# Kernel tuning notes

Hardware: AMD Instinct MI355X
Metric: run time of the kernel (lower is better)

## Reference

```python
import jax, jax.numpy as jnp
import numpy as np
from jax import lax

LENGTH, WIDTH = 64, 64
INPUT_DIM = 1


def _convlstm_layer(x_tbchw, W, b):
    """Run one ConvLSTM layer over time. x_tbchw: (L,B,Cin,H,W).
    W: (4*hid, Cin+hid, 3, 3), b: (4*hid,). Returns (outputs (L,B,hid,H,W), last_h)."""
    L, B, _, H, Wd = x_tbchw.shape
    hid = W.shape[0] // 4
    h0 = jnp.zeros((B, hid, H, Wd), dtype=x_tbchw.dtype)
    c0 = jnp.zeros((B, hid, H, Wd), dtype=x_tbchw.dtype)

    def step(carry, xt):
        h, c = carry
        z = lax.conv_general_dilated(
            jnp.concatenate([xt, h], axis=1), W,
            window_strides=(1, 1), padding='SAME',
            dimension_numbers=('NCHW', 'OIHW', 'NCHW'))
        z = z + b[None, :, None, None]
        cc_i, cc_f, cc_o, cc_g = jnp.split(z, 4, axis=1)
        c_next = jax.nn.sigmoid(cc_f) * c + jax.nn.sigmoid(cc_i) * jnp.tanh(cc_g)
        h_next = jax.nn.sigmoid(cc_o) * jnp.tanh(c_next)
        return (h_next, c_next), h_next

    (h_last, _), outs = lax.scan(step, (h0, c0), x_tbchw)
    return outs, h_last


def setup_inputs() -> dict:
    key = jax.random.key(0)
    k1, k2, k3 = jax.random.split(key, 3)
    B, L, N = 16, 12, LENGTH * WIDTH
    emd, out_len = 128, 12
    return {
        'history_data': jax.random.normal(k1, (B, L, N, 1), dtype=jnp.float32),
        'future_data': jnp.zeros((B, L, N, 1), dtype=jnp.float32),
        'W0': jax.random.normal(k2, (4 * emd, INPUT_DIM + emd, 3, 3), dtype=jnp.float32) * 0.05,
        'b0': jnp.zeros((4 * emd,), dtype=jnp.float32),
        'W1': jax.random.normal(k3, (4 * out_len, emd + out_len, 3, 3), dtype=jnp.float32) * 0.05,
        'b1': jnp.zeros((4 * out_len,), dtype=jnp.float32),
        'batch_seen': 0,
        'epoch': 0,
        'train': 1,
    }


def reference(history_data, future_data, W0, b0, W1, b1, batch_seen, epoch, train):
    B, L, N, C = history_data.shape
    # (B,L,1,H,W) -> (L,B,1,H,W) for time-major scan
    x = history_data[..., :INPUT_DIM].reshape(B, L, INPUT_DIM, LENGTH, WIDTH)
    x = jnp.transpose(x, (1, 0, 2, 3, 4))
    outs0, _ = _convlstm_layer(x, W0, b0)          # (L,B,emd,H,W)
    _, h_last = _convlstm_layer(outs0, W1, b1)     # (B,out_len,H,W)
    prediction = h_last.reshape(B, L, LENGTH * WIDTH)[..., None]  # (B,L,N,1)
    return prediction
```

## Files before the change

kernel.cpp:

```cpp
#include <hip/hip_runtime.h>
#include <hip/hip_bf16.h>


typedef __attribute__((ext_vector_type(8))) short short8;
typedef __attribute__((ext_vector_type(4))) float float4v;

#define CS 160
#define KTOT 1440
#define RSTR 2560
#define BSTR 10240

__device__ __forceinline__ float sigf(float x) { return 1.f / (1.f + __expf(-x)); }
__device__ __forceinline__ short f2hs(float v) {
  _Float16 h = (_Float16)v;
  return *(short*)&h;
}
__device__ __forceinline__ float bs2f(short s) {
  __hip_bfloat16 h; *(short*)&h = s; return __bfloat162float(h);
}
__device__ __forceinline__ short f2bs(float v) {
  __hip_bfloat16 h = __float2bfloat16(v);
  return *(short*)&h;
}

__device__ __forceinline__ void async_ld16(const short* g, short* l) {
  __builtin_amdgcn_global_load_lds(
      (const __attribute__((address_space(1))) unsigned int*)g,
      (__attribute__((address_space(3))) unsigned int*)l, 16, 0, 0);
}

__device__ __forceinline__ void stage_one(const short* __restrict__ rowPtr, bool rowOK,
                                          short* dstRow, int lane,
                                          const short* __restrict__ zp, int j) {
  int e = j * 64 + lane;
  int px = e >> 2, v = e & 3;
  int xx = px - 1;
  bool ok = rowOK && (px < 66) && (xx >= 0) && (xx < 64);
  const short* g = ok ? (rowPtr + (size_t)xx * CS + v * 8) : zp;
  async_ld16(g, dstRow + e * 8);
}

__device__ __forceinline__ void stage_row(const short* __restrict__ rowPtr, bool rowOK,
                                          short* dstRow, int lane,
                                          const short* __restrict__ zp) {
  #pragma unroll
  for (int j = 0; j < 5; ++j) stage_one(rowPtr, rowOK, dstRow, lane, zp, j);
}

__global__ void detect_dtype(const unsigned short* __restrict__ w0, int* __restrict__ flag) {
  int lane = threadIdx.x;
  int cnt = 0;
  for (int i = 0; i < 4; ++i) {
    unsigned short u = w0[2 * (lane + 64 * i)];
    int e = (u >> 7) & 0xFF;
    unsigned long long b = __ballot(e >= 0xC0);
    cnt += __popcll(b);
  }
  if (lane == 0) *flag = (cnt > 32) ? 1 : 0;
}

__global__ void canon_x(const void* __restrict__ hist, short* __restrict__ Xc,
                        const int* __restrict__ flag) {
  int i = blockIdx.x * 256 + threadIdx.x;
  float v = (*flag) ? ((const float*)hist)[i] : bs2f(((const short*)hist)[i]);
  if (!isfinite(v) || fabsf(v) > 1e4f) v = 0.f;
  Xc[i] = f2hs(v);
}

__global__ void canon_b(const void* __restrict__ b0, const void* __restrict__ b1,
                        float* __restrict__ Bc0, float* __restrict__ Bc1,
                        const int* __restrict__ flag) {
  int i = blockIdx.x * 256 + threadIdx.x;
  int fl = *flag;
  if (i < 512) {
    float v = fl ? ((const float*)b0)[i] : bs2f(((const short*)b0)[i]);
    if (!isfinite(v) || fabsf(v) > 1e4f) v = 0.f;
    Bc0[i] = v;
  } else if (i < 560) {
    int j = i - 512;
    float v = fl ? ((const float*)b1)[j] : bs2f(((const short*)b1)[j]);
    if (!isfinite(v) || fabsf(v) > 1e4f) v = 0.f;
    Bc1[j] = v;
  }
}

__global__ void prep_w0(const void* __restrict__ W0, short* __restrict__ Wp,
                        const int* __restrict__ flag) {
  int i = blockIdx.x * 256 + threadIdx.x;
  if (i >= 512 * KTOT) return;
  int fl = *flag;
  int co = i / KTOT, k = i - co * KTOT;
  int tap = k / CS, c = k - tap * CS;
  int ci = -1;
  if (c == 0) ci = 0;
  else if (c <= 128) ci = c;
  float w = 0.f;
  if (ci >= 0) {
    int widx = (co * 129 + ci) * 9 + tap;
    w = fl ? ((const float*)W0)[widx] : bs2f(((const short*)W0)[widx]);
    if (!isfinite(w) || fabsf(w) > 1e4f) w = 0.f;
  }
  Wp[i] = f2hs(w);
}

__global__ void prep_w1(const void* __restrict__ W1, short* __restrict__ Wp,
                        const int* __restrict__ flag) {
  int i = blockIdx.x * 256 + threadIdx.x;
  if (i >= 48 * KTOT) return;
  int fl = *flag;
  int co = i / KTOT, k = i - co * KTOT;
  int tap = k / CS, c = k - tap * CS;
  int ci = -1;
  if (c >= 1 && c <= 140) ci = c - 1;
  float w = 0.f;
  if (ci >= 0) {
    int widx = (co * 140 + ci) * 9 + tap;
    w = fl ? ((const float*)W1)[widx] : bs2f(((const short*)W1)[widx]);
    if (!isfinite(w) || fabsf(w) > 1e4f) w = 0.f;
  }
  Wp[i] = f2hs(w);
}

__global__ void fill_x0(const short* __restrict__ Xc, short* __restrict__ P0) {
  int p = blockIdx.x * 256 + threadIdx.x;
  int b = p >> 12, pix = p & 4095;
  P0[(size_t)p * CS] = Xc[b * 12 * 4096 + pix];
}

__global__ __launch_bounds__(256, 2) void gemm_gate0(
    const short* __restrict__ Pcur, short* __restrict__ Pnext,
    const short* __restrict__ Wp, const float* __restrict__ Bc0,
    float* __restrict__ C0, const short* __restrict__ Xc,
    const short* __restrict__ zp, int t) {
  int pbx = blockIdx.x;
  int xcd = pbx & 7, i = pbx >> 3;
  int mt = xcd * 64 + (i & 63);
  int nt = i >> 6;
  int b = mt >> 5, y0 = (mt & 31) * 2;
  int tid = threadIdx.x, wave = tid >> 6, lane = tid & 63;
  int ln15 = lane & 15, quad = lane >> 4;
  int wm = wave & 1, wn = wave >> 1;
  int hc = nt * 32 + wn * 16 + ln15;

  __shared__ __align__(16) short halo[2 * BSTR];

  float4v acc[4][4];
  #pragma unroll
  for (int i2 = 0; i2 < 4; ++i2)
    #pragma unroll
    for (int j = 0; j < 4; ++j) acc[i2][j] = (float4v){0.f, 0.f, 0.f, 0.f};

  const short* wbase = Wp + (size_t)hc * KTOT + quad * 8;
  short8 bcur[4], bnxt[4];
  #pragma unroll
  for (int g = 0; g < 4; ++g)
    bcur[g] = *(const short8*)(wbase + (size_t)g * 128 * KTOT);

  int yy = y0 - 1 + wave;
  bool rowOK = (yy >= 0) && (yy < 64);
  const short* rowBase = Pcur + (size_t)((b * 64 + yy) * 64) * CS;

  stage_row(rowBase, rowOK, halo + wave * RSTR, lane, zp);
  __syncthreads();

  for (int ch = 0; ch < 5; ++ch) {
    int c0 = ch * 32;
    const short* cur = halo + (ch & 1) * BSTR;
    short* nxtDst = halo + ((ch + 1) & 1) * BSTR + wave * RSTR;
    const short* nxtSrc = rowBase + c0 + 32;
    #pragma unroll
    for (int tap = 0; tap < 9; ++tap) {
      int dy = tap / 3, dx = tap - dy * 3;
      if (ch < 4 && tap < 5)
        stage_one(nxtSrc, rowOK, nxtDst, lane, zp, tap);
      int ntap = (tap < 8) ? tap + 1 : 0;
      int nc0 = (tap < 8) ? c0 : ((ch < 4) ? c0 + 32 : c0);
      #pragma unroll
      for (int g = 0; g < 4; ++g)
        bnxt[g] = *(const short8*)(wbase + (size_t)g * 128 * KTOT + ntap * CS + nc0);

      short8 af[4];
      #pragma unroll
      for (int mf = 0; mf < 4; ++mf)
        af[mf] = *(const short8*)&cur[(wm + dy) * RSTR + (mf * 16 + ln15 + dx) * 32 + quad * 8];
      #pragma unroll
      for (int g = 0; g < 4; ++g)
        #pragma unroll
        for (int mf = 0; mf < 4; ++mf)
          acc[mf][g] = __builtin_amdgcn_mfma_f32_16x16x32_f16(af[mf], bcur[g], acc[mf][g], 0, 0, 0);
      #pragma unroll
      for (int g = 0; g < 4; ++g) bcur[g] = bnxt[g];
    }
    __syncthreads();
  }

  float bi = Bc0[hc], bff = Bc0[128 + hc], bo = Bc0[256 + hc], bg = Bc0[384 + hc];
  int rowPix = (b * 64 + y0 + wm) * 64;
  #pragma unroll
  for (int mf = 0; mf < 4; ++mf) {
    #pragma unroll
    for (int r = 0; r < 4; ++r) {
      int x = mf * 16 + quad * 4 + r;
      int pix = rowPix + x;
      float zi = acc[mf][0][r] + bi;
      float zf = acc[mf][1][r] + bff;
      float zo = acc[mf][2][r] + bo;
      float zg = acc[mf][3][r] + bg;
      float cprev = C0[(size_t)pix * 128 + hc];
      float cn = sigf(zf) * cprev + sigf(zi) * tanhf(zg);
      float hn = sigf(zo) * tanhf(cn);
      C0[(size_t)pix * 128 + hc] = cn;
      Pnext[(size_t)pix * CS + 1 + hc] = f2hs(hn);
    }
  }
  if (nt == 0 && t < 11 && tid < 128) {
    int rr = tid >> 6, x = tid & 63;
    int yw = y0 + rr;
    Pnext[(size_t)((b * 64 + yw) * 64 + x) * CS] = Xc[(b * 12 + t + 1) * 4096 + yw * 64 + x];
  }
}

__global__ __launch_bounds__(256, 2) void gemm_gate1(
    const short* __restrict__ Prd, short* __restrict__ Pwr,
    const short* __restrict__ Wp, const float* __restrict__ Bc1,
    float* __restrict__ C1, void* __restrict__ outp,
    const short* __restrict__ zp, const int* __restrict__ flagp, int t) {
  int pbx = blockIdx.x;
  int bid = (pbx & 7) * 64 + (pbx >> 3);
  int b = bid >> 5, y0 = (bid & 31) * 2;
  int tid = threadIdx.x, wave = tid >> 6, lane = tid & 63;
  int ln15 = lane & 15, quad = lane >> 4;
  int wr = wave >> 1, wh = wave & 1;
  int flagv = *flagp;

  __shared__ __align__(16) short halo[2 * BSTR];

  float4v acc[2][3];
  #pragma unroll
  for (int i = 0; i < 2; ++i)
    #pragma unroll
    for (int j = 0; j < 3; ++j) acc[i][j] = (float4v){0.f, 0.f, 0.f, 0.f};

  int yy = y0 - 1 + wave;
  bool rowOK = (yy >= 0) && (yy < 64);
  const short* rowBase = Prd + (size_t)((b * 64 + yy) * 64) * CS;

  const short* wbase = Wp + (size_t)ln15 * KTOT + quad * 8;
  short8 bcur[3], bnxt[3];
  #pragma unroll
  for (int nf = 0; nf < 3; ++nf)
    bcur[nf] = *(const short8*)(wbase + (size_t)nf * 16 * KTOT);

  stage_row(rowBase, rowOK, halo + wave * RSTR, lane, zp);
  __syncthreads();

  for (int ch = 0; ch < 5; ++ch) {
    int c0 = ch * 32;
    const short* cur = halo + (ch & 1) * BSTR;
    short* nxtDst = halo + ((ch + 1) & 1) * BSTR + wave * RSTR;
    const short* nxtSrc = rowBase + c0 + 32;
    #pragma unroll
    for (int tap = 0; tap < 9; ++tap) {
      int dy = tap / 3, dx = tap - dy * 3;
      if (ch < 4 && tap < 5)
        stage_one(nxtSrc, rowOK, nxtDst, lane, zp, tap);
      int ntap = (tap < 8) ? tap + 1 : 0;
      int nc0 = (tap < 8) ? c0 : ((ch < 4) ? c0 + 32 : c0);
      #pragma unroll
      for (int nf = 0; nf < 3; ++nf)
        bnxt[nf] = *(const short8*)(wbase + (size_t)nf * 16 * KTOT + ntap * CS + nc0);

      short8 af[2];
      #pragma unroll
      for (int mf = 0; mf < 2; ++mf)
        af[mf] = *(const short8*)&cur[(wr + dy) * RSTR + (wh * 32 + mf * 16 + ln15 + dx) * 32
                                      + quad * 8];
      #pragma unroll
      for (int nf = 0; nf < 3; ++nf)
        #pragma unroll
        for (int mf = 0; mf < 2; ++mf)
          acc[mf][nf] = __builtin_amdgcn_mfma_f32_16x16x32_f16(af[mf], bcur[nf], acc[mf][nf], 0, 0, 0);
      #pragma unroll
      for (int nf = 0; nf < 3; ++nf) bcur[nf] = bnxt[nf];
    }
    __syncthreads();
  }

  float* zbuf = (float*)halo;
  #pragma unroll
  for (int mf = 0; mf < 2; ++mf)
    #pragma unroll
    for (int nf = 0; nf < 3; ++nf)
      #pragma unroll
      for (int r = 0; r < 4; ++r) {
        int pxl = wr * 64 + wh * 32 + mf * 16 + quad * 4 + r;
        zbuf[pxl * 48 + nf * 16 + ln15] = acc[mf][nf][r];
      }
  __syncthreads();

  #pragma unroll
  for (int k = 0; k < 6; ++k) {
    int id = k * 256 + tid;
    int hc = id >> 7, pxl = id & 127;
    float zi = zbuf[pxl * 48 + hc]      + Bc1[hc];
    float zf = zbuf[pxl * 48 + 12 + hc] + Bc1[12 + hc];
    float zo = zbuf[pxl * 48 + 24 + hc] + Bc1[24 + hc];
    float zg = zbuf[pxl * 48 + 36 + hc] + Bc1[36 + hc];
    int y = y0 + (pxl >> 6), x = pxl & 63;
    int pix = (b * 64 + y) * 64 + x;
    float cprev = C1[(size_t)pix * 12 + hc];
    float cn = sigf(zf) * cprev + sigf(zi) * tanhf(zg);
    float hn = sigf(zo) * tanhf(cn);
    C1[(size_t)pix * 12 + hc] = cn;
    Pwr[(size_t)pix * CS + 129 + hc] = f2hs(hn);
    if (t == 11) {
      int oidx = (b * 12 + hc) * 4096 + y * 64 + x;
      if (flagv) ((float*)outp)[oidx] = hn;
      else ((short*)outp)[oidx] = f2bs(hn);
    }
  }
}

extern "C" void kernel_launch(void* const* d_in, const int* in_sizes, int n_in,
                              void* d_out, int out_size, void* d_ws, size_t ws_size,
                              hipStream_t stream) {
  const void* hist = d_in[0];
  const void* W0 = d_in[2];
  const void* b0 = d_in[3];
  const void* W1 = d_in[4];
  const void* b1 = d_in[5];

  char* ws = (char*)d_ws;
  const size_t PszB = (size_t)16 * 4096 * CS * 2;
  short* P[2] = {(short*)ws, (short*)(ws + PszB)};
  float* C0 = (float*)(ws + 2 * PszB);
  const size_t C0e = 2 * PszB + 33554432;
  float* C1 = (float*)(ws + C0e);
  const size_t C1e = C0e + 3145728;
  short* zp = (short*)(ws + C1e);
  const size_t zpe = C1e + 256;
  short* Xc = (short*)(ws + zpe);
  const size_t Xce = zpe + 1572864;
  short* Wp0 = (short*)(ws + Xce);
  const size_t W0e = Xce + (size_t)512 * KTOT * 2;
  short* Wp1 = (short*)(ws + W0e);
  const size_t W1e = W0e + (size_t)48 * KTOT * 2;
  float* Bc0 = (float*)(ws + W1e);
  float* Bc1 = (float*)(ws + W1e + 2048);
  int* flag = (int*)(ws + W1e + 2048 + 192);

  hipMemsetAsync(ws, 0, zpe, stream);
  detect_dtype<<<1, 64, 0, stream>>>((const unsigned short*)W0, flag);
  canon_x<<<3072, 256, 0, stream>>>(hist, Xc, flag);
  canon_b<<<3, 256, 0, stream>>>(b0, b1, Bc0, Bc1, flag);
  prep_w0<<<(512 * KTOT + 255) / 256, 256, 0, stream>>>(W0, Wp0, flag);
  prep_w1<<<(48 * KTOT + 255) / 256, 256, 0, stream>>>(W1, Wp1, flag);
  fill_x0<<<256, 256, 0, stream>>>(Xc, P[0]);

  for (int t = 0; t < 12; ++t) {
    gemm_gate0<<<2048, 256, 0, stream>>>(P[t & 1], P[(t + 1) & 1], Wp0, Bc0, C0, Xc, zp, t);
    gemm_gate1<<<512, 256, 0, stream>>>(P[(t + 1) & 1], P[t & 1], Wp1, Bc1, C1,
                                        d_out, zp, flag, t);
  }
}
```

Measured before the change: 2.090 ms.

## Enlarge gate0 tile to four output rows per block, halving grid

Each gate0 block now computes four image rows instead of two, staging a six-row halo in LDS (up from four) and keeping eight M-fragments of accumulators per wave. This halves the grid and the redundant halo loads per output row, and doubles reuse of each loaded weight fragment across MFMAs. In exchange it doubles the accumulator registers and raises LDS use, which can reduce occupancy or cause spills under the 256,2 launch bounds.

Measured after the change: 2.060 ms. About the same (-1.4%).

```diff
diff --git a/kernel.cpp b/kernel.cpp
--- a/kernel.cpp
+++ b/kernel.cpp
@@ -9,6 +9,7 @@
 #define KTOT 1440
 #define RSTR 2560
 #define BSTR 10240
+#define BSTR6 15360
 
 __device__ __forceinline__ float sigf(float x) { return 1.f / (1.f + __expf(-x)); }
 __device__ __forceinline__ short f2hs(float v) {
@@ -134,19 +135,19 @@
     const short* __restrict__ zp, int t) {
   int pbx = blockIdx.x;
   int xcd = pbx & 7, i = pbx >> 3;
-  int mt = xcd * 64 + (i & 63);
-  int nt = i >> 6;
-  int b = mt >> 5, y0 = (mt & 31) * 2;
+  int mt = xcd * 32 + (i & 31);
+  int nt = i >> 5;
+  int b = mt >> 4, y0 = (mt & 15) * 4;
   int tid = threadIdx.x, wave = tid >> 6, lane = tid & 63;
   int ln15 = lane & 15, quad = lane >> 4;
   int wm = wave & 1, wn = wave >> 1;
   int hc = nt * 32 + wn * 16 + ln15;
 
-  __shared__ __align__(16) short halo[2 * BSTR];
-
-  float4v acc[4][4];
-  #pragma unroll
-  for (int i2 = 0; i2 < 4; ++i2)
+  __shared__ __align__(16) short halo[2 * BSTR6];
+
+  float4v acc[8][4];
+  #pragma unroll
+  for (int i2 = 0; i2 < 8; ++i2)
     #pragma unroll
     for (int j = 0; j < 4; ++j) acc[i2][j] = (float4v){0.f, 0.f, 0.f, 0.f};
 
@@ -156,37 +157,45 @@
   for (int g = 0; g < 4; ++g)
     bcur[g] = *(const short8*)(wbase + (size_t)g * 128 * KTOT);
 
-  int yy = y0 - 1 + wave;
-  bool rowOK = (yy >= 0) && (yy < 64);
-  const short* rowBase = Pcur + (size_t)((b * 64 + yy) * 64) * CS;
-
-  stage_row(rowBase, rowOK, halo + wave * RSTR, lane, zp);
+  int yyA = y0 - 1 + wave;
+  bool okA = (yyA >= 0) && (yyA < 64);
+  const short* baseA = Pcur + (size_t)((b * 64 + yyA) * 64) * CS;
+  int yyB = y0 + 3 + wave;
+  bool okB = (wave < 2) && (yyB < 64);
+  const short* baseB = Pcur + (size_t)((b * 64 + yyB) * 64) * CS;
+
+  stage_row(baseA, okA, halo + wave * RSTR, lane, zp);
+  if (wave < 2) stage_row(baseB, okB, halo + (4 + wave) * RSTR, lane, zp);
   __syncthreads();
 
   for (int ch = 0; ch < 5; ++ch) {
     int c0 = ch * 32;
-    const short* cur = halo + (ch & 1) * BSTR;
-    short* nxtDst = halo + ((ch + 1) & 1) * BSTR + wave * RSTR;
-    const short* nxtSrc = rowBase + c0 + 32;
+    const short* cur = halo + (ch & 1) * BSTR6;
+    short* nd = halo + ((ch + 1) & 1) * BSTR6;
+    const short* srcA = baseA + c0 + 32;
+    const short* srcB = baseB + c0 + 32;
     #pragma unroll
     for (int tap = 0; tap < 9; ++tap) {
       int dy = tap / 3, dx = tap - dy * 3;
-      if (ch < 4 && tap < 5)
-        stage_one(nxtSrc, rowOK, nxtDst, lane, zp, tap);
+      if (ch < 4 && tap < 5) {
+        stage_one(srcA, okA, nd + wave * RSTR, lane, zp, tap);
+        if (wave < 2) stage_one(srcB, okB, nd + (4 + wave) * RSTR, lane, zp, tap);
+      }
       int ntap = (tap < 8) ? tap + 1 : 0;
       int nc0 = (tap < 8) ? c0 : ((ch < 4) ? c0 + 32 : c0);
       #pragma unroll
       for (int g = 0; g < 4; ++g)
         bnxt[g] = *(const short8*)(wbase + (size_t)g * 128 * KTOT + ntap * CS + nc0);
 
-      short8 af[4];
-      #pragma unroll
-      for (int mf = 0; mf < 4; ++mf)
-        af[mf] = *(const short8*)&cur[(wm + dy) * RSTR + (mf * 16 + ln15 + dx) * 32 + quad * 8];
+      short8 af[8];
+      #pragma unroll
+      for (int mf = 0; mf < 8; ++mf)
+        af[mf] = *(const short8*)&cur[(wm * 2 + (mf >> 2) + dy) * RSTR
+                                      + ((mf & 3) * 16 + ln15 + dx) * 32 + quad * 8];
       #pragma unroll
       for (int g = 0; g < 4; ++g)
         #pragma unroll
-        for (int mf = 0; mf < 4; ++mf)
+        for (int mf = 0; mf < 8; ++mf)
           acc[mf][g] = __builtin_amdgcn_mfma_f32_16x16x32_f16(af[mf], bcur[g], acc[mf][g], 0, 0, 0);
       #pragma unroll
       for (int g = 0; g < 4; ++g) bcur[g] = bnxt[g];
@@ -195,13 +204,14 @@
   }
 
   float bi = Bc0[hc], bff = Bc0[128 + hc], bo = Bc0[256 + hc], bg = Bc0[384 + hc];
-  int rowPix = (b * 64 + y0 + wm) * 64;
-  #pragma unroll
-  for (int mf = 0; mf < 4; ++mf) {
+  #pragma unroll
+  for (int mf = 0; mf < 8; ++mf) {
+    int row = y0 + wm * 2 + (mf >> 2);
+    int pixRow = (b * 64 + row) * 64;
     #pragma unroll
     for (int r = 0; r < 4; ++r) {
-      int x = mf * 16 + quad * 4 + r;
-      int pix = rowPix + x;
+      int x = (mf & 3) * 16 + quad * 4 + r;
+      int pix = pixRow + x;
       float zi = acc[mf][0][r] + bi;
       float zf = acc[mf][1][r] + bff;
       float zo = acc[mf][2][r] + bo;
@@ -213,7 +223,7 @@
       Pnext[(size_t)pix * CS + 1 + hc] = f2hs(hn);
     }
   }
-  if (nt == 0 && t < 11 && tid < 128) {
+  if (nt == 0 && t < 11) {
     int rr = tid >> 6, x = tid & 63;
     int yw = y0 + rr;
     Pnext[(size_t)((b * 64 + yw) * 64 + x) * CS] = Xc[(b * 12 + t + 1) * 4096 + yw * 64 + x];
@@ -358,7 +368,7 @@
   fill_x0<<<256, 256, 0, stream>>>(Xc, P[0]);
 
   for (int t = 0; t < 12; ++t) {
-    gemm_gate0<<<2048, 256, 0, stream>>>(P[t & 1], P[(t + 1) & 1], Wp0, Bc0, C0, Xc, zp, t);
+    gemm_gate0<<<1024, 256, 0, stream>>>(P[t & 1], P[(t + 1) & 1], Wp0, Bc0, C0, Xc, zp, t);
     gemm_gate1<<<512, 256, 0, stream>>>(P[(t + 1) & 1], P[t & 1], Wp1, Bc1, C1,
                                         d_out, zp, flag, t);
   }
```
